# Performance work log

Measured on AMD Instinct MI355X. Metric: run time of the kernel, lower is better.

Reference implementation:

```python
import jax, jax.numpy as jnp
import numpy as np

K = 16  # neighbors per node

def setup_inputs() -> dict:
    key = jax.random.key(0)
    feature = jax.random.normal(key, (16384, 512), dtype=jnp.float32)
    return {"feature": feature, "k": K}

def reference(feature, k):
    # cosine-normalize rows (eps added to norm, matching torch)
    nrm = jnp.linalg.norm(feature, axis=-1, keepdims=True)
    fn = feature / (nrm + 1e-10)
    sim = fn @ fn.T                      # [N, N]
    n = sim.shape[0]
    # zero the diagonal (sim - diag_embed(diag(sim)))
    sim = sim - jnp.diag(jnp.diag(sim))
    _, idx = jax.lax.top_k(sim, k)       # [N, k]
    row = jnp.repeat(jnp.arange(n), k)   # [N*k]
    col = idx.reshape(-1)
    edge_index = jnp.stack([row, col], axis=0).astype(jnp.int64)
    return edge_index
```

## Files before the change

kernel.cpp:

```cpp
#include <hip/hip_runtime.h>
#include <hip/hip_fp16.h>
#include <math.h>

#define NN   16384
#define DD   512
#define KNN  16
#define CAND 32
#define STRIPW 4096
#define NSTRIP (NN / STRIPW)
#define KT2  64
#define LDK  72

typedef __attribute__((ext_vector_type(8))) short bf16x8;
typedef __attribute__((ext_vector_type(4))) float f32x4;

__global__ __launch_bounds__(256) void norm_kernel(const float* __restrict__ feat,
                                                   float* __restrict__ nrm) {
#pragma clang fp contract(off)
    const int t   = threadIdx.x;
    const int row = blockIdx.x * 64 + (t >> 2);
    const int bid = t & 3;
    const float4* p4 = (const float4*)(feat + (size_t)row * DD + bid * 128);
    float r[4][4];
    #pragma unroll
    for (int m = 0; m < 4; m++) {
        float4 q = p4[m];
        r[m][0] = q.x * q.x; r[m][1] = q.y * q.y;
        r[m][2] = q.z * q.z; r[m][3] = q.w * q.w;
    }
    #pragma unroll
    for (int tt = 1; tt < 8; tt++) {
        #pragma unroll
        for (int m = 0; m < 4; m++) {
            float4 q = p4[tt * 4 + m];
            r[m][0] += q.x * q.x; r[m][1] += q.y * q.y;
            r[m][2] += q.z * q.z; r[m][3] += q.w * q.w;
        }
    }
    float v0 = (r[0][0] + r[1][0]) + (r[2][0] + r[3][0]);
    float v1 = (r[0][1] + r[1][1]) + (r[2][1] + r[3][1]);
    float v2 = (r[0][2] + r[1][2]) + (r[2][2] + r[3][2]);
    float v3 = (r[0][3] + r[1][3]) + (r[2][3] + r[3][3]);
    float B  = (v0 + v1) + (v2 + v3);
    B += __shfl_xor(B, 1, 64);
    B += __shfl_xor(B, 2, 64);
    if (bid == 0) nrm[row] = sqrtf(B) + 1e-10f;
}

__device__ inline ushort bf16rne(float f) {
    unsigned u = __float_as_uint(f);
    u += 0x7fffu + ((u >> 16) & 1u);
    return (ushort)(u >> 16);
}
__global__ __launch_bounds__(256) void fn_kernel(const float* __restrict__ feat,
                                                 const float* __restrict__ nrm,
                                                 float* __restrict__ fn,
                                                 ushort* __restrict__ fnb) {
    int i4  = blockIdx.x * 256 + threadIdx.x;
    int row = i4 >> 7;
    float n = nrm[row];
    float4 v = ((const float4*)feat)[i4];
    float4 o = make_float4(v.x / n, v.y / n, v.z / n, v.w / n);
    ((float4*)fn)[i4] = o;
    ushort4 b = {bf16rne(o.x), bf16rne(o.y), bf16rne(o.z), bf16rne(o.w)};
    ((ushort4*)fnb)[i4] = b;
}

__global__ __launch_bounds__(256) void gemm_kernel(const ushort* __restrict__ fnb,
                                                   int stripBase,
                                                   __half* __restrict__ simS) {
    __shared__ ushort As[128][LDK];
    __shared__ ushort Bs[128][LDK];
    const int t    = threadIdx.x;
    const int wave = t >> 6, lane = t & 63;
    const int rbase = blockIdx.y * 128;
    const int cbL   = blockIdx.x * 128;
    const int wr = (wave >> 1) * 64, wc = (wave & 1) * 64;
    const int m = lane & 15, quad = lane >> 4;
    const int srow = t >> 1, shalf = (t & 1) * 32;

    f32x4 acc[4][4];
    #pragma unroll
    for (int i = 0; i < 4; i++)
        #pragma unroll
        for (int j = 0; j < 4; j++) acc[i][j] = (f32x4){0.f, 0.f, 0.f, 0.f};

    const ushort* arow = fnb + (size_t)(rbase + srow) * DD + shalf;
    const ushort* brow = fnb + (size_t)(stripBase + cbL + srow) * DD + shalf;

    for (int kb = 0; kb < DD; kb += KT2) {
        __syncthreads();
        #pragma unroll
        for (int j = 0; j < 4; j++) {
            *(int4*)&As[srow][shalf + j * 8] = *(const int4*)(arow + kb + j * 8);
            *(int4*)&Bs[srow][shalf + j * 8] = *(const int4*)(brow + kb + j * 8);
        }
        __syncthreads();

        #pragma unroll
        for (int ks = 0; ks < KT2; ks += 32) {
            bf16x8 af[4], bv[4];
            #pragma unroll
            for (int i = 0; i < 4; i++)
                af[i] = *(const bf16x8*)&As[wr + i * 16 + m][ks + quad * 8];
            #pragma unroll
            for (int j = 0; j < 4; j++)
                bv[j] = *(const bf16x8*)&Bs[wc + j * 16 + m][ks + quad * 8];
            #pragma unroll
            for (int i = 0; i < 4; i++)
                #pragma unroll
                for (int j = 0; j < 4; j++)
                    acc[i][j] = __builtin_amdgcn_mfma_f32_16x16x32_bf16(
                        af[i], bv[j], acc[i][j], 0, 0, 0);
        }
    }
    #pragma unroll
    for (int i = 0; i < 4; i++)
        #pragma unroll
        for (int j = 0; j < 4; j++)
            #pragma unroll
            for (int r = 0; r < 4; r++) {
                int grow = rbase + wr + i * 16 + quad * 4 + r;
                int gcol = cbL + wc + j * 16 + m;
                simS[(size_t)grow * STRIPW + gcol] = __float2half(acc[i][j][r]);
            }
}

__global__ __launch_bounds__(256) void select_kernel(const __half* __restrict__ simS,
                                                     int stripBase, int firstStrip,
                                                     float* __restrict__ lval,
                                                     int* __restrict__ lidx) {
    const int lane = threadIdx.x & 63;
    const int row  = blockIdx.x * 4 + (threadIdx.x >> 6);
    float lv; int li;
    if (firstStrip) { lv = -3.4e38f; li = 0x7fffffff; }
    else {
        lv = (lane < CAND) ? lval[(size_t)row * CAND + lane] : -3.4e38f;
        li = (lane < CAND) ? lidx[(size_t)row * CAND + lane] : 0x7fffffff;
    }
    const __half* sp = simS + (size_t)row * STRIPW;
    for (int it = 0; it < STRIPW / 64; it++) {
        int   c = stripBase + it * 64 + lane;
        float v = __half2float(sp[it * 64 + lane]);
        float vmin = __shfl(lv, CAND - 1);
        int   imin = __shfl(li, CAND - 1);
        bool adm = ((v > vmin) || (v == vmin && c < imin)) && (c != row);
        unsigned long long mask = __ballot(adm);
        while (mask) {
            int src = __builtin_ctzll(mask); mask &= mask - 1;
            float bvv = __shfl(v, src);
            int   bc  = stripBase + it * 64 + src;
            bool better = (lv > bvv) || (lv == bvv && li < bc);
            unsigned long long bb = __ballot(better) & ((1ull << CAND) - 1);
            int p = __popcll(bb);
            if (p < CAND) {
                float pv = __shfl_up(lv, 1);
                int   pi = __shfl_up(li, 1);
                float nlv = (lane < p) ? lv : (lane == p ? bvv : pv);
                int   nli = (lane < p) ? li : (lane == p ? bc : pi);
                if (lane < CAND) { lv = nlv; li = nli; }
            }
        }
    }
    if (lane < CAND) {
        lval[(size_t)row * CAND + lane] = lv;
        lidx[(size_t)row * CAND + lane] = li;
    }
}

__global__ __launch_bounds__(256) void rescore_kernel(const float* __restrict__ fn,
                                                      const int* __restrict__ lidx,
                                                      int* __restrict__ out) {
    __shared__ float sv[8][CAND];
    __shared__ int   si[8][CAND];
    const int w    = threadIdx.x >> 5;
    const int lane = threadIdx.x & 31;
    const int row  = blockIdx.x * 8 + w;
    const int c = lidx[(size_t)row * CAND + lane];
    const float* q = fn + (size_t)row * DD;
    const float* p = fn + (size_t)c * DD;
    float s = 0.0f;
    for (int k = 0; k < DD; k += 4) {
        float4 qv = *(const float4*)(q + k);
        float4 pv = *(const float4*)(p + k);
        s = __builtin_fmaf(qv.x, pv.x, s);
        s = __builtin_fmaf(qv.y, pv.y, s);
        s = __builtin_fmaf(qv.z, pv.z, s);
        s = __builtin_fmaf(qv.w, pv.w, s);
    }
    sv[w][lane] = s;
    si[w][lane] = c;
    __syncthreads();
    int rank = 0;
    #pragma unroll 8
    for (int mm = 0; mm < CAND; mm++) {
        float vm = sv[w][mm];
        rank += (vm > s) || (vm == s && si[w][mm] < c);
    }
    if (rank < KNN) {
        out[(size_t)row * KNN + rank]            = row;
        out[(size_t)NN * KNN + row * KNN + rank] = c;
    }
}

#define MT 64
#define CT 128
#define KT 32
#define SIM_LD 132
template <bool PRE>
__global__ __launch_bounds__(256) void knn_exact_kernel(const float* __restrict__ src,
                                                        const float* __restrict__ nrm,
                                                        int* __restrict__ out) {
    __shared__ union {
        struct { float As[KT][MT]; float Bs[KT][CT]; } stage;
        float sim[MT][SIM_LD];
    } u;
    __shared__ float tval[MT][KNN];
    __shared__ int   tidx[MT][KNN];
    const int t  = threadIdx.x;
    const int r0 = blockIdx.x * MT;
    const int tx = t & 15;
    const int ty = t >> 4;
    for (int i = t; i < MT * KNN; i += 256) {
        ((float*)tval)[i] = -3.4e38f;
        ((int*)tidx)[i]   = 0;
    }
    const int arow = t >> 2, akq = t & 3;
    const int bcol = t >> 1, bkh = t & 1;
    for (int ct = 0; ct < NN / CT; ct++) {
        const int c0 = ct * CT;
        float acc[4][8];
        #pragma unroll
        for (int rr = 0; rr < 4; rr++)
            #pragma unroll
            for (int cc = 0; cc < 8; cc++) acc[rr][cc] = 0.0f;
        for (int kt = 0; kt < DD / KT; kt++) {
            const int kb = kt * KT;
            __syncthreads();
            {
                const float* ap = src + (size_t)(r0 + arow) * DD + kb + akq * 8;
                float4 a0 = *(const float4*)ap;
                float4 a1 = *(const float4*)(ap + 4);
                if (!PRE) {
                    float nA = nrm[r0 + arow];
                    a0.x /= nA; a0.y /= nA; a0.z /= nA; a0.w /= nA;
                    a1.x /= nA; a1.y /= nA; a1.z /= nA; a1.w /= nA;
                }
                int k0 = akq * 8;
                u.stage.As[k0 + 0][arow] = a0.x; u.stage.As[k0 + 1][arow] = a0.y;
                u.stage.As[k0 + 2][arow] = a0.z; u.stage.As[k0 + 3][arow] = a0.w;
                u.stage.As[k0 + 4][arow] = a1.x; u.stage.As[k0 + 5][arow] = a1.y;
                u.stage.As[k0 + 6][arow] = a1.z; u.stage.As[k0 + 7][arow] = a1.w;
            }
            {
                const float* bp = src + (size_t)(c0 + bcol) * DD + kb + bkh * 16;
                float4 b0 = *(const float4*)bp;
                float4 b1 = *(const float4*)(bp + 4);
                float4 b2 = *(const float4*)(bp + 8);
                float4 b3 = *(const float4*)(bp + 12);
                if (!PRE) {
                    float nB = nrm[c0 + bcol];
                    b0.x /= nB; b0.y /= nB; b0.z /= nB; b0.w /= nB;
                    b1.x /= nB; b1.y /= nB; b1.z /= nB; b1.w /= nB;
                    b2.x /= nB; b2.y /= nB; b2.z /= nB; b2.w /= nB;
                    b3.x /= nB; b3.y /= nB; b3.z /= nB; b3.w /= nB;
                }
                int k0 = bkh * 16;
                u.stage.Bs[k0 +  0][bcol] = b0.x; u.stage.Bs[k0 +  1][bcol] = b0.y;
                u.stage.Bs[k0 +  2][bcol] = b0.z; u.stage.Bs[k0 +  3][bcol] = b0.w;
                u.stage.Bs[k0 +  4][bcol] = b1.x; u.stage.Bs[k0 +  5][bcol] = b1.y;
                u.stage.Bs[k0 +  6][bcol] = b1.z; u.stage.Bs[k0 +  7][bcol] = b1.w;
                u.stage.Bs[k0 +  8][bcol] = b2.x; u.stage.Bs[k0 +  9][bcol] = b2.y;
                u.stage.Bs[k0 + 10][bcol] = b2.z; u.stage.Bs[k0 + 11][bcol] = b2.w;
                u.stage.Bs[k0 + 12][bcol] = b3.x; u.stage.Bs[k0 + 13][bcol] = b3.y;
                u.stage.Bs[k0 + 14][bcol] = b3.z; u.stage.Bs[k0 + 15][bcol] = b3.w;
            }
            __syncthreads();
            #pragma unroll
            for (int kk = 0; kk < KT; kk++) {
                float4 av  = *(const float4*)&u.stage.As[kk][ty * 4];
                float4 bv0 = *(const float4*)&u.stage.Bs[kk][tx * 4];
                float4 bv1 = *(const float4*)&u.stage.Bs[kk][64 + tx * 4];
                float ar[4] = {av.x, av.y, av.z, av.w};
                float br[8] = {bv0.x, bv0.y, bv0.z, bv0.w,
                               bv1.x, bv1.y, bv1.z, bv1.w};
                #pragma unroll
                for (int rr = 0; rr < 4; rr++)
                    #pragma unroll
                    for (int cc = 0; cc < 8; cc++)
                        acc[rr][cc] = __builtin_fmaf(ar[rr], br[cc], acc[rr][cc]);
            }
        }
        __syncthreads();
        {
            #pragma unroll
            for (int rr = 0; rr < 4; rr++) {
                *(float4*)&u.sim[ty * 4 + rr][tx * 4] =
                    make_float4(acc[rr][0], acc[rr][1], acc[rr][2], acc[rr][3]);
                *(float4*)&u.sim[ty * 4 + rr][64 + tx * 4] =
                    make_float4(acc[rr][4], acc[rr][5], acc[rr][6], acc[rr][7]);
            }
        }
        __syncthreads();
        if ((t & 3) == 0) {
            const int lr = t >> 2, grow = r0 + lr;
            float vmin = tval[lr][KNN - 1];
            for (int j = 0; j < CT / 4; j++) {
                float4 v4 = *(const float4*)&u.sim[lr][j * 4];
                float vs[4] = {v4.x, v4.y, v4.z, v4.w};
                #pragma unroll
                for (int e = 0; e < 4; e++) {
                    int cc2 = c0 + j * 4 + e;
                    float v = vs[e];
                    if (cc2 == grow) continue;
                    if (v > vmin) {
                        int p = KNN - 1;
                        while (p > 0 && tval[lr][p - 1] < v) {
                            tval[lr][p] = tval[lr][p - 1];
                            tidx[lr][p] = tidx[lr][p - 1];
                            p--;
                        }
                        tval[lr][p] = v;
                        tidx[lr][p] = cc2;
                        vmin = tval[lr][KNN - 1];
                    }
                }
            }
        }
    }
    __syncthreads();
    for (int i = t; i < MT * KNN; i += 256) {
        int lr = i / KNN, j = i % KNN;
        int grow = r0 + lr;
        out[(size_t)grow * KNN + j]            = grow;
        out[(size_t)NN * KNN + grow * KNN + j] = tidx[lr][j];
    }
}

extern "C" void kernel_launch(void* const* d_in, const int* in_sizes, int n_in,
                              void* d_out, int out_size, void* d_ws, size_t ws_size,
                              hipStream_t stream) {
    const float* feat = (const float*)d_in[0];
    int* out = (int*)d_out;
    char* ws = (char*)d_ws;

    const size_t oNrm  = 0;
    const size_t oFn   = 64 * 1024;
    const size_t oFnb  = oFn  + (size_t)NN * DD * 4;
    const size_t oLv   = oFnb + (size_t)NN * DD * 2;
    const size_t oLi   = oLv  + (size_t)NN * CAND * 4;
    const size_t oSim  = oLi  + (size_t)NN * CAND * 4;
    const size_t need  = oSim + (size_t)NN * STRIPW * 2;
    float*  nrm  = (float*)(ws + oNrm);
    float*  fn   = (float*)(ws + oFn);
    ushort* fnb  = (ushort*)(ws + oFnb);
    float*  lval = (float*)(ws + oLv);
    int*    lidx = (int*)(ws + oLi);
    __half* simS = (__half*)(ws + oSim);

    norm_kernel<<<NN / 64, 256, 0, stream>>>(feat, nrm);

    if (ws_size >= need) {
        fn_kernel<<<(NN * DD / 4) / 256, 256, 0, stream>>>(feat, nrm, fn, fnb);
        for (int s = 0; s < NSTRIP; s++) {
            dim3 ggrid(STRIPW / 128, NN / 128);
            gemm_kernel<<<ggrid, 256, 0, stream>>>(fnb, s * STRIPW, simS);
            select_kernel<<<NN / 4, 256, 0, stream>>>(simS, s * STRIPW, s == 0,
                                                      lval, lidx);
        }
        rescore_kernel<<<NN / 8, 256, 0, stream>>>(fn, lidx, out);
    } else if (ws_size >= oFn + (size_t)NN * DD * 4) {
        fn_kernel<<<(NN * DD / 4) / 256, 256, 0, stream>>>(feat, nrm, fn,
                                                           (ushort*)(ws + oFn));
        knn_exact_kernel<true><<<NN / MT, 256, 0, stream>>>(fn, nrm, out);
    } else {
        knn_exact_kernel<false><<<NN / MT, 256, 0, stream>>>(feat, nrm, out);
    }
}
```

Measured before the change: 1.005 ms.

## Use direct global-to-LDS swizzled loads, half2 select, smaller candidate list

The GEMM tile loads now go straight from global memory into LDS through global_load_lds, using an XOR-swizzled layout in place of the padded shared arrays, so register staging and LDS bank conflicts are avoided. The select kernel reads two fp16 similarities per lane as half2, halving the number of load and ballot iterations. The candidate list shrinks from 32 to 24, which cuts insertion and rescore work but leaves less margin for bf16/fp16 rounding to push a true neighbor out before the exact fp32 rescore. The rescore loop is also unrolled further.

New measurement: 881.0 us. 1.14x faster.

```diff
diff --git a/kernel.cpp b/kernel.cpp
--- a/kernel.cpp
+++ b/kernel.cpp
@@ -5,14 +5,19 @@
 #define NN   16384
 #define DD   512
 #define KNN  16
-#define CAND 32
+#define CAND 24
 #define STRIPW 4096
 #define NSTRIP (NN / STRIPW)
-#define KT2  64
-#define LDK  72
 
 typedef __attribute__((ext_vector_type(8))) short bf16x8;
 typedef __attribute__((ext_vector_type(4))) float f32x4;
+typedef unsigned int u32;
+
+__device__ __forceinline__ void load16_lds(const ushort* g, void* l) {
+    __builtin_amdgcn_global_load_lds(
+        (const __attribute__((address_space(1))) u32*)(const void*)g,
+        (__attribute__((address_space(3))) u32*)l, 16, 0, 0);
+}
 
 __global__ __launch_bounds__(256) void norm_kernel(const float* __restrict__ feat,
                                                    float* __restrict__ nrm) {
@@ -69,15 +74,16 @@
 __global__ __launch_bounds__(256) void gemm_kernel(const ushort* __restrict__ fnb,
                                                    int stripBase,
                                                    __half* __restrict__ simS) {
-    __shared__ ushort As[128][LDK];
-    __shared__ ushort Bs[128][LDK];
+    __shared__ ushort As[128 * 64];
+    __shared__ ushort Bs[128 * 64];
     const int t    = threadIdx.x;
     const int wave = t >> 6, lane = t & 63;
     const int rbase = blockIdx.y * 128;
     const int cbL   = blockIdx.x * 128;
     const int wr = (wave >> 1) * 64, wc = (wave & 1) * 64;
     const int m = lane & 15, quad = lane >> 4;
-    const int srow = t >> 1, shalf = (t & 1) * 32;
+    const int rseg = lane >> 3;
+    const int cchk = (lane & 7) ^ rseg;
 
     f32x4 acc[4][4];
     #pragma unroll
@@ -85,27 +91,32 @@
         #pragma unroll
         for (int j = 0; j < 4; j++) acc[i][j] = (f32x4){0.f, 0.f, 0.f, 0.f};
 
-    const ushort* arow = fnb + (size_t)(rbase + srow) * DD + shalf;
-    const ushort* brow = fnb + (size_t)(stripBase + cbL + srow) * DD + shalf;
-
-    for (int kb = 0; kb < DD; kb += KT2) {
+    const int swz = ((m & 7) << 4);
+
+    for (int kb = 0; kb < DD; kb += 64) {
         __syncthreads();
         #pragma unroll
-        for (int j = 0; j < 4; j++) {
-            *(int4*)&As[srow][shalf + j * 8] = *(const int4*)(arow + kb + j * 8);
-            *(int4*)&Bs[srow][shalf + j * 8] = *(const int4*)(brow + kb + j * 8);
+        for (int q = 0; q < 4; q++) {
+            int s   = wave * 4 + q;
+            int row = s * 8 + rseg;
+            const ushort* ga = fnb + (size_t)(rbase + row) * DD + kb + cchk * 8;
+            const ushort* gb = fnb + (size_t)(stripBase + cbL + row) * DD + kb + cchk * 8;
+            load16_lds(ga, (char*)As + s * 1024);
+            load16_lds(gb, (char*)Bs + s * 1024);
         }
         __syncthreads();
 
         #pragma unroll
-        for (int ks = 0; ks < KT2; ks += 32) {
+        for (int ks = 0; ks < 64; ks += 32) {
+            const int cb16 = (ks >> 3) + quad;
+            const int off  = ((cb16 << 4) ^ swz);
             bf16x8 af[4], bv[4];
             #pragma unroll
             for (int i = 0; i < 4; i++)
-                af[i] = *(const bf16x8*)&As[wr + i * 16 + m][ks + quad * 8];
+                af[i] = *(const bf16x8*)((const char*)As + (wr + i * 16 + m) * 128 + off);
             #pragma unroll
             for (int j = 0; j < 4; j++)
-                bv[j] = *(const bf16x8*)&Bs[wc + j * 16 + m][ks + quad * 8];
+                bv[j] = *(const bf16x8*)((const char*)Bs + (wc + j * 16 + m) * 128 + off);
             #pragma unroll
             for (int i = 0; i < 4; i++)
                 #pragma unroll
@@ -126,7 +137,7 @@
             }
 }
 
-__global__ __launch_bounds__(256) void select_kernel(const __half* __restrict__ simS,
+__global__ __launch_bounds__(256) void select_kernel(const __half2* __restrict__ simS2,
                                                      int stripBase, int firstStrip,
                                                      float* __restrict__ lval,
                                                      int* __restrict__ lidx) {
@@ -138,27 +149,34 @@
         lv = (lane < CAND) ? lval[(size_t)row * CAND + lane] : -3.4e38f;
         li = (lane < CAND) ? lidx[(size_t)row * CAND + lane] : 0x7fffffff;
     }
-    const __half* sp = simS + (size_t)row * STRIPW;
-    for (int it = 0; it < STRIPW / 64; it++) {
-        int   c = stripBase + it * 64 + lane;
-        float v = __half2float(sp[it * 64 + lane]);
+    const __half2* sp = simS2 + (size_t)row * (STRIPW / 2);
+    for (int it = 0; it < STRIPW / 128; it++) {
+        __half2 h = sp[it * 64 + lane];
+        float v0 = __low2float(h), v1 = __high2float(h);
+        int c0 = stripBase + it * 128 + lane * 2, c1 = c0 + 1;
         float vmin = __shfl(lv, CAND - 1);
         int   imin = __shfl(li, CAND - 1);
-        bool adm = ((v > vmin) || (v == vmin && c < imin)) && (c != row);
-        unsigned long long mask = __ballot(adm);
-        while (mask) {
-            int src = __builtin_ctzll(mask); mask &= mask - 1;
-            float bvv = __shfl(v, src);
-            int   bc  = stripBase + it * 64 + src;
-            bool better = (lv > bvv) || (lv == bvv && li < bc);
-            unsigned long long bb = __ballot(better) & ((1ull << CAND) - 1);
-            int p = __popcll(bb);
-            if (p < CAND) {
-                float pv = __shfl_up(lv, 1);
-                int   pi = __shfl_up(li, 1);
-                float nlv = (lane < p) ? lv : (lane == p ? bvv : pv);
-                int   nli = (lane < p) ? li : (lane == p ? bc : pi);
-                if (lane < CAND) { lv = nlv; li = nli; }
+        bool a0 = ((v0 > vmin) || (v0 == vmin && c0 < imin)) && (c0 != row);
+        bool a1 = ((v1 > vmin) || (v1 == vmin && c1 < imin)) && (c1 != row);
+        unsigned long long m0 = __ballot(a0), m1 = __ballot(a1);
+        #pragma unroll
+        for (int ph = 0; ph < 2; ph++) {
+            unsigned long long mask = ph ? m1 : m0;
+            float vv = ph ? v1 : v0;
+            while (mask) {
+                int src = __builtin_ctzll(mask); mask &= mask - 1;
+                float bvv = __shfl(vv, src);
+                int   bc  = stripBase + it * 128 + src * 2 + ph;
+                bool better = (lv > bvv) || (lv == bvv && li < bc);
+                unsigned long long bb = __ballot(better) & ((1ull << CAND) - 1);
+                int p = __popcll(bb);
+                if (p < CAND) {
+                    float pv = __shfl_up(lv, 1);
+                    int   pi = __shfl_up(li, 1);
+                    float nlv = (lane < p) ? lv : (lane == p ? bvv : pv);
+                    int   nli = (lane < p) ? li : (lane == p ? bc : pi);
+                    if (lane < CAND) { lv = nlv; li = nli; }
+                }
             }
         }
     }
@@ -176,30 +194,38 @@
     const int w    = threadIdx.x >> 5;
     const int lane = threadIdx.x & 31;
     const int row  = blockIdx.x * 8 + w;
-    const int c = lidx[(size_t)row * CAND + lane];
+    const bool valid = lane < CAND;
+    const int c = valid ? lidx[(size_t)row * CAND + lane] : 0;
     const float* q = fn + (size_t)row * DD;
     const float* p = fn + (size_t)c * DD;
     float s = 0.0f;
-    for (int k = 0; k < DD; k += 4) {
-        float4 qv = *(const float4*)(q + k);
-        float4 pv = *(const float4*)(p + k);
-        s = __builtin_fmaf(qv.x, pv.x, s);
-        s = __builtin_fmaf(qv.y, pv.y, s);
-        s = __builtin_fmaf(qv.z, pv.z, s);
-        s = __builtin_fmaf(qv.w, pv.w, s);
-    }
-    sv[w][lane] = s;
-    si[w][lane] = c;
+    for (int k = 0; k < DD; k += 16) {
+        float4 q0 = *(const float4*)(q + k),      p0 = *(const float4*)(p + k);
+        float4 q1 = *(const float4*)(q + k + 4),  p1 = *(const float4*)(p + k + 4);
+        float4 q2 = *(const float4*)(q + k + 8),  p2 = *(const float4*)(p + k + 8);
+        float4 q3 = *(const float4*)(q + k + 12), p3 = *(const float4*)(p + k + 12);
+        s = __builtin_fmaf(q0.x, p0.x, s); s = __builtin_fmaf(q0.y, p0.y, s);
+        s = __builtin_fmaf(q0.z, p0.z, s); s = __builtin_fmaf(q0.w, p0.w, s);
+        s = __builtin_fmaf(q1.x, p1.x, s); s = __builtin_fmaf(q1.y, p1.y, s);
+        s = __builtin_fmaf(q1.z, p1.z, s); s = __builtin_fmaf(q1.w, p1.w, s);
+        s = __builtin_fmaf(q2.x, p2.x, s); s = __builtin_fmaf(q2.y, p2.y, s);
+        s = __builtin_fmaf(q2.z, p2.z, s); s = __builtin_fmaf(q2.w, p2.w, s);
+        s = __builtin_fmaf(q3.x, p3.x, s); s = __builtin_fmaf(q3.y, p3.y, s);
+        s = __builtin_fmaf(q3.z, p3.z, s); s = __builtin_fmaf(q3.w, p3.w, s);
+    }
+    if (valid) { sv[w][lane] = s; si[w][lane] = c; }
     __syncthreads();
-    int rank = 0;
-    #pragma unroll 8
-    for (int mm = 0; mm < CAND; mm++) {
-        float vm = sv[w][mm];
-        rank += (vm > s) || (vm == s && si[w][mm] < c);
-    }
-    if (rank < KNN) {
-        out[(size_t)row * KNN + rank]            = row;
-        out[(size_t)NN * KNN + row * KNN + rank] = c;
+    if (valid) {
+        int rank = 0;
+        #pragma unroll 8
+        for (int mm = 0; mm < CAND; mm++) {
+            float vm = sv[w][mm];
+            rank += (vm > s) || (vm == s && si[w][mm] < c);
+        }
+        if (rank < KNN) {
+            out[(size_t)row * KNN + rank]            = row;
+            out[(size_t)NN * KNN + row * KNN + rank] = c;
+        }
     }
 }
 
@@ -365,7 +391,8 @@
         for (int s = 0; s < NSTRIP; s++) {
             dim3 ggrid(STRIPW / 128, NN / 128);
             gemm_kernel<<<ggrid, 256, 0, stream>>>(fnb, s * STRIPW, simS);
-            select_kernel<<<NN / 4, 256, 0, stream>>>(simS, s * STRIPW, s == 0,
+            select_kernel<<<NN / 4, 256, 0, stream>>>((const __half2*)simS,
+                                                      s * STRIPW, s == 0,
                                                       lval, lidx);
         }
         rescore_kernel<<<NN / 8, 256, 0, stream>>>(fn, lidx, out);
```
